# Kernel optimization log

Hardware: AMD Instinct MI355X
Metric: run time of the kernel (lower is better)

Reference implementation:

```python
import jax, jax.numpy as jnp
import numpy as np

D, H, DH, R = 1024, 16, 64, 32          # embed, heads, head_dim, per-head attn rank
R_OUT, I, R_FC1, R_FC2 = 512, 4096, 512, 512
B, S = 2, 2048
EPS = 1e-5


def _layernorm(x, w, b):
    m = jnp.mean(x, axis=-1, keepdims=True)
    v = jnp.mean(jnp.square(x - m), axis=-1, keepdims=True)
    return (x - m) * jax.lax.rsqrt(v + EPS) * w + b


def setup_inputs() -> dict:
    key = jax.random.key(0)
    ks = jax.random.split(key, 24)
    n = lambda i, shape, s: (jax.random.normal(ks[i], shape, jnp.float32) * s)
    return {
        'hidden_states': jax.random.normal(ks[0], (B, S, D), jnp.float32),
        'attention_mask': jnp.ones((B, S), dtype=bool),
        'ln1_w': jnp.ones((D,), jnp.float32), 'ln1_b': jnp.zeros((D,), jnp.float32),
        'q_U': n(1, (D, H, R), 0.02), 'q_V': n(2, (H, R, DH), 0.1), 'q_b': jnp.zeros((H, DH), jnp.float32),
        'k_U': n(3, (D, H, R), 0.02), 'k_V': n(4, (H, R, DH), 0.1), 'k_b': jnp.zeros((H, DH), jnp.float32),
        'v_U': n(5, (D, H, R), 0.02), 'v_V': n(6, (H, R, DH), 0.1), 'v_b': jnp.zeros((H, DH), jnp.float32),
        'out_U': n(7, (D, R_OUT), 0.02), 'out_V': n(8, (R_OUT, D), 0.02), 'out_b': jnp.zeros((D,), jnp.float32),
        'ln2_w': jnp.ones((D,), jnp.float32), 'ln2_b': jnp.zeros((D,), jnp.float32),
        'fc1_U': n(9, (D, R_FC1), 0.02), 'fc1_V': n(10, (R_FC1, I), 0.02), 'fc1_b': jnp.zeros((I,), jnp.float32),
        'fc2_U': n(11, (I, R_FC2), 0.02), 'fc2_V': n(12, (R_FC2, D), 0.02), 'fc2_b': jnp.zeros((D,), jnp.float32),
    }


def _forward(hidden_states, attention_mask, ln1_w, ln1_b, q_U, q_V, q_b, k_U, k_V, k_b,
             v_U, v_V, v_b, out_U, out_V, out_b, ln2_w, ln2_b,
             fc1_U, fc1_V, fc1_b, fc2_U, fc2_V, fc2_b):
    b, s, d = hidden_states.shape
    x = _layernorm(hidden_states, ln1_w, ln1_b)
    # low-rank per-head projections: P = x U  (bhsr), then Q = P V + b
    Pq = jnp.einsum('bsd,dhr->bhsr', x, q_U)
    Pk = jnp.einsum('bsd,dhr->bhsr', x, k_U)
    Pv = jnp.einsum('bsd,dhr->bhsr', x, v_U)
    Q = jnp.einsum('bhsr,hre->bhse', Pq, q_V) + q_b[None, :, None, :]
    K = jnp.einsum('bhsr,hre->bhse', Pk, k_V) + k_b[None, :, None, :]
    V = jnp.einsum('bhsr,hre->bhse', Pv, v_V) + v_b[None, :, None, :]
    scale = 1.0 / jnp.sqrt(jnp.asarray(DH, Q.dtype))
    scores = jnp.einsum('bhse,bhte->bhst', Q, K) * scale
    causal = jnp.tril(jnp.ones((s, s), dtype=bool))
    keymask = attention_mask[:, None, None, :]  # [B,1,1,S] key padding mask
    mask = jnp.logical_and(causal[None, None], keymask)
    scores = jnp.where(mask, scores, jnp.asarray(-1e9, scores.dtype))
    P = jax.nn.softmax(scores, axis=-1)
    Y = jnp.einsum('bhst,bhte->bhse', P, V)           # [B,H,S,dh]
    Y = Y.transpose(0, 2, 1, 3).reshape(b, s, d)       # [B,S,D]
    Y = (Y @ out_U) @ out_V + out_b                    # low-rank out-proj
    h = hidden_states + Y
    z = _layernorm(h, ln2_w, ln2_b)
    t1 = z @ fc1_U                                     # [B,S,r_fc1]
    a = jax.nn.gelu(t1 @ fc1_V + fc1_b, approximate=True)
    h2 = (a @ fc2_U) @ fc2_V + fc2_b
    return h + h2


def reference(hidden_states, attention_mask, ln1_w, ln1_b, q_U, q_V, q_b, k_U, k_V, k_b,
              v_U, v_V, v_b, out_U, out_V, out_b, ln2_w, ln2_b,
              fc1_U, fc1_V, fc1_b, fc2_U, fc2_V, fc2_b):
    return _forward(hidden_states, attention_mask, ln1_w, ln1_b, q_U, q_V, q_b,
                    k_U, k_V, k_b, v_U, v_V, v_b, out_U, out_V, out_b,
                    ln2_w, ln2_b, fc1_U, fc1_V, fc1_b, fc2_U, fc2_V, fc2_b)
```

## Files before the change

kernel.cpp:

```cpp
#include <hip/hip_runtime.h>
#include <math.h>

constexpr int Bc = 2, Sc = 2048, Dc = 1024, Hc = 16, DHc = 64, Rc = 32;
constexpr int Nt = Bc * Sc;
constexpr int NP3 = 1536;

typedef __attribute__((ext_vector_type(8))) short bf16x8;
typedef __attribute__((ext_vector_type(4))) float f32x4;

__device__ __forceinline__ unsigned short f2bf(float f) {
  unsigned u = __float_as_uint(f);
  u += 0x7fffu + ((u >> 16) & 1u);
  return (unsigned short)(u >> 16);
}
__device__ __forceinline__ float bf2f(unsigned short h) {
  return __uint_as_float(((unsigned)h) << 16);
}

#define GLOAD_LDS16(gp, lp)                                                    \
  __builtin_amdgcn_global_load_lds(                                            \
      (const __attribute__((address_space(1))) void*)(gp),                     \
      (__attribute__((address_space(3))) void*)(lp), 16, 0, 0)

__global__ __launch_bounds__(256) void ln_kernel(
    const float* __restrict__ X, const float* __restrict__ w,
    const float* __restrict__ b, unsigned short* __restrict__ Out) {
  int row = blockIdx.x;
  const float* x = X + (size_t)row * Dc;
  unsigned short* o = Out + (size_t)row * Dc;
  int tid = threadIdx.x;
  float4 v = ((const float4*)x)[tid];
  float s  = v.x + v.y + v.z + v.w;
  float sq = v.x * v.x + v.y * v.y + v.z * v.z + v.w * v.w;
#pragma unroll
  for (int off = 32; off; off >>= 1) {
    s  += __shfl_down(s, off);
    sq += __shfl_down(sq, off);
  }
  __shared__ float rs[4], rq[4];
  int wid = tid >> 6, lane = tid & 63;
  if (lane == 0) { rs[wid] = s; rq[wid] = sq; }
  __syncthreads();
  float ts = rs[0] + rs[1] + rs[2] + rs[3];
  float tq = rq[0] + rq[1] + rq[2] + rq[3];
  float mean = ts * (1.f / Dc);
  float var  = tq * (1.f / Dc) - mean * mean;
  float rstd = rsqrtf(var + 1e-5f);
  float4 wv = ((const float4*)w)[tid];
  float4 bv = ((const float4*)b)[tid];
  ushort4 ov;
  ov.x = f2bf((v.x - mean) * rstd * wv.x + bv.x);
  ov.y = f2bf((v.y - mean) * rstd * wv.y + bv.y);
  ov.z = f2bf((v.z - mean) * rstd * wv.z + bv.z);
  ov.w = f2bf((v.w - mean) * rstd * wv.w + bv.w);
  ((ushort4*)o)[tid] = ov;
}

__global__ __launch_bounds__(256) void transpose_cvt(
    const float* __restrict__ in, unsigned short* __restrict__ out,
    int R, int C) {
  __shared__ float t[32][33];
  int tx = threadIdx.x & 31, ty = threadIdx.x >> 5;
  int r0 = blockIdx.y * 32, c0 = blockIdx.x * 32;
#pragma unroll
  for (int i = 0; i < 4; ++i)
    t[ty + i * 8][tx] = in[(size_t)(r0 + ty + i * 8) * C + c0 + tx];
  __syncthreads();
#pragma unroll
  for (int i = 0; i < 4; ++i)
    out[(size_t)(c0 + ty + i * 8) * R + r0 + tx] = f2bf(t[tx][ty + i * 8]);
}

__global__ __launch_bounds__(256) void transpose_hd(
    const unsigned short* __restrict__ in, unsigned short* __restrict__ out) {
  __shared__ unsigned short t[32][33];
  int bh = blockIdx.z;
  int s0 = blockIdx.x * 32, e0 = blockIdx.y * 32;
  int tx = threadIdx.x & 31, ty = threadIdx.x >> 5;
  const unsigned short* ib = in + ((size_t)bh * Sc + s0) * 64 + e0;
  unsigned short* ob = out + ((size_t)bh * 64 + e0) * Sc + s0;
#pragma unroll
  for (int i = 0; i < 4; ++i)
    t[ty + i * 8][tx] = ib[(size_t)(ty + i * 8) * 64 + tx];
  __syncthreads();
#pragma unroll
  for (int i = 0; i < 4; ++i)
    ob[(size_t)(ty + i * 8) * Sc + tx] = t[tx][ty + i * 8];
}

__device__ __forceinline__ float gelu_f(float v) {
  float c = v + 0.044715f * v * v * v;
  return 0.5f * v * (1.f + tanhf(0.7978845608028654f * c));
}

template <bool OBF16, int ACT, bool BIAS, bool RES>
__global__ __launch_bounds__(256) void gemm_bf(
    const unsigned short* __restrict__ A, const unsigned short* __restrict__ BT,
    const float* __restrict__ bias, const float* __restrict__ res,
    void* __restrict__ Cv, int M, int N, int K) {
  __shared__ unsigned short As[128 * 32];
  __shared__ unsigned short Bs[128 * 32];
  int tid = threadIdx.x;
  int lane = tid & 63, wv = tid >> 6;
  int bm = blockIdx.y * 128, bn = blockIdx.x * 128;
  int wr = wv >> 1, wc = wv & 1;
  f32x4 acc[4][4] = {};
  int soff0 = wv * 512 + lane * 8;
  int soff1 = soff0 + 2048;
  int ar0 = soff0 >> 5, ak0 = soff0 & 31;
  int ar1 = soff1 >> 5, ak1 = soff1 & 31;
  const unsigned short* Ab = A + (size_t)bm * K;
  const unsigned short* Bb = BT + (size_t)bn * K;
  for (int k0 = 0; k0 < K; k0 += 32) {
    __syncthreads();
    GLOAD_LDS16(Ab + (size_t)ar0 * K + k0 + ak0, As + wv * 512);
    GLOAD_LDS16(Ab + (size_t)ar1 * K + k0 + ak1, As + 2048 + wv * 512);
    GLOAD_LDS16(Bb + (size_t)ar0 * K + k0 + ak0, Bs + wv * 512);
    GLOAD_LDS16(Bb + (size_t)ar1 * K + k0 + ak1, Bs + 2048 + wv * 512);
    __syncthreads();
    bf16x8 af[4], bf[4];
#pragma unroll
    for (int m = 0; m < 4; ++m)
      af[m] = *(const bf16x8*)&As[(wr * 64 + m * 16 + (lane & 15)) * 32 + (lane >> 4) * 8];
#pragma unroll
    for (int n = 0; n < 4; ++n)
      bf[n] = *(const bf16x8*)&Bs[(wc * 64 + n * 16 + (lane & 15)) * 32 + (lane >> 4) * 8];
#pragma unroll
    for (int m = 0; m < 4; ++m)
#pragma unroll
      for (int n = 0; n < 4; ++n)
        acc[m][n] = __builtin_amdgcn_mfma_f32_16x16x32_bf16(af[m], bf[n], acc[m][n], 0, 0, 0);
  }
  int cg = lane >> 4;
#pragma unroll
  for (int m = 0; m < 4; ++m) {
#pragma unroll
    for (int n = 0; n < 4; ++n) {
      int row0 = bm + wr * 64 + m * 16 + cg * 4;
      int col  = bn + wc * 64 + n * 16 + (lane & 15);
      float bb = BIAS ? bias[col] : 0.f;
#pragma unroll
      for (int i = 0; i < 4; ++i) {
        float v = acc[m][n][i];
        if (BIAS) v += bb;
        if (ACT == 1) v = gelu_f(v);
        if (RES) v += res[(size_t)(row0 + i) * N + col];
        if (OBF16)
          ((unsigned short*)Cv)[(size_t)(row0 + i) * N + col] = f2bf(v);
        else
          ((float*)Cv)[(size_t)(row0 + i) * N + col] = v;
      }
    }
  }
}

__global__ __launch_bounds__(256) void pv_kernel(
    const unsigned short* __restrict__ P, const float* __restrict__ Vw,
    const float* __restrict__ bias, unsigned short* __restrict__ Out,
    int colOff) {
  int idx = blockIdx.x * 256 + threadIdx.x;
  int e = idx & 63;
  int h = (idx >> 6) & 15;
  int n = idx >> 10;
  const unsigned short* prow = P + (size_t)n * NP3 + colOff + h * Rc;
  const float* vcol = Vw + h * (Rc * DHc) + e;
  float acc = 0.f;
#pragma unroll
  for (int r = 0; r < Rc; ++r) acc = fmaf(bf2f(prow[r]), vcol[r * DHc], acc);
  acc += bias[(h << 6) + e];
  int b = n / Sc, s = n % Sc;
  Out[(((size_t)(b * Hc + h) * Sc + s) << 6) + e] = f2bf(acc);
}

__global__ __launch_bounds__(256) void attn_kernel(
    const unsigned short* __restrict__ Q, const unsigned short* __restrict__ K,
    const unsigned short* __restrict__ VT, unsigned short* __restrict__ Y) {
  __shared__ unsigned short Ks[64 * 64];
  __shared__ unsigned short Vs[64 * 64];
  __shared__ unsigned short Ps[4][16 * 64];
  int bid = blockIdx.x;
  int bh = bid >> 5;
  int qt = 31 - (bid & 31);
  int qbase = qt * 64;
  int tid = threadIdx.x, lane = tid & 63, w = tid >> 6;
  int g = lane >> 4, c = lane & 15;
  const unsigned short* Qg = Q + (size_t)bh * Sc * 64;
  const unsigned short* Kg = K + (size_t)bh * Sc * 64;
  const unsigned short* Vg = VT + (size_t)bh * 64 * Sc;
  int q0 = qbase + w * 16;
  bf16x8 qa0 = *(const bf16x8*)(Qg + (size_t)(q0 + c) * 64 + g * 8);
  bf16x8 qa1 = *(const bf16x8*)(Qg + (size_t)(q0 + c) * 64 + 32 + g * 8);
  f32x4 O0 = {0.f, 0.f, 0.f, 0.f}, O1 = O0, O2 = O0, O3 = O0;
  float m[4] = {-1e30f, -1e30f, -1e30f, -1e30f};
  float l[4] = {0.f, 0.f, 0.f, 0.f};
  int r0s = tid >> 3;
  int b0s = (tid & 7) ^ (r0s & 7);
  int r1s = (256 + tid) >> 3;
  int b1s = (tid & 7) ^ (r1s & 7);
  size_t kOff0 = (size_t)r0s * 64 + b0s * 8;
  size_t kOff1 = (size_t)r1s * 64 + b1s * 8;
  size_t vOff0 = (size_t)r0s * Sc + b0s * 8;
  size_t vOff1 = (size_t)r1s * Sc + b1s * 8;
  unsigned short* KsD0 = Ks + w * 512;
  unsigned short* KsD1 = Ks + 2048 + w * 512;
  unsigned short* VsD0 = Vs + w * 512;
  unsigned short* VsD1 = Vs + 2048 + w * 512;
  unsigned short* Pw = Ps[w];
  const f32x4 zero = {0.f, 0.f, 0.f, 0.f};
  int swc = c & 7;

  for (int kt = 0; kt <= qt; ++kt) {
    __syncthreads();
    {
      const unsigned short* Kt = Kg + (size_t)kt * 64 * 64;
      const unsigned short* Vt = Vg + (size_t)kt * 64;
      GLOAD_LDS16(Kt + kOff0, KsD0);
      GLOAD_LDS16(Kt + kOff1, KsD1);
      GLOAD_LDS16(Vt + vOff0, VsD0);
      GLOAD_LDS16(Vt + vOff1, VsD1);
    }
    __syncthreads();
    f32x4 sA[4];
#pragma unroll
    for (int kb = 0; kb < 4; ++kb) {
      int keyr = kb * 16 + c;
      int sw = keyr & 7;
      bf16x8 k0 = *(const bf16x8*)&Ks[keyr * 64 + ((g ^ sw) << 3)];
      bf16x8 k1 = *(const bf16x8*)&Ks[keyr * 64 + (((4 + g) ^ sw) << 3)];
      f32x4 a = __builtin_amdgcn_mfma_f32_16x16x32_bf16(qa0, k0, zero, 0, 0, 0);
      a = __builtin_amdgcn_mfma_f32_16x16x32_bf16(qa1, k1, a, 0, 0, 0);
      sA[kb] = a;
    }
    float p[4][4], rm[4];
#pragma unroll
    for (int i = 0; i < 4; ++i) rm[i] = -1e30f;
#pragma unroll
    for (int kb = 0; kb < 4; ++kb)
#pragma unroll
      for (int i = 0; i < 4; ++i) {
        float s = sA[kb][i] * 0.125f;
        if (kt == qt && (kb * 16 + c) > (w * 16 + 4 * g + i)) s = -1e30f;
        p[kb][i] = s;
        rm[i] = fmaxf(rm[i], s);
      }
#pragma unroll
    for (int i = 0; i < 4; ++i) {
      rm[i] = fmaxf(rm[i], __shfl_xor(rm[i], 1));
      rm[i] = fmaxf(rm[i], __shfl_xor(rm[i], 2));
      rm[i] = fmaxf(rm[i], __shfl_xor(rm[i], 4));
      rm[i] = fmaxf(rm[i], __shfl_xor(rm[i], 8));
    }
    float sc[4], ls[4];
#pragma unroll
    for (int i = 0; i < 4; ++i) {
      float mn = fmaxf(m[i], rm[i]);
      sc[i] = __expf(m[i] - mn);
      m[i] = mn;
      ls[i] = 0.f;
    }
#pragma unroll
    for (int kb = 0; kb < 4; ++kb)
#pragma unroll
      for (int i = 0; i < 4; ++i) {
        float e = __expf(p[kb][i] - m[i]);
        p[kb][i] = e;
        ls[i] += e;
      }
#pragma unroll
    for (int i = 0; i < 4; ++i) {
      ls[i] += __shfl_xor(ls[i], 1);
      ls[i] += __shfl_xor(ls[i], 2);
      ls[i] += __shfl_xor(ls[i], 4);
      ls[i] += __shfl_xor(ls[i], 8);
      l[i] = l[i] * sc[i] + ls[i];
      O0[i] *= sc[i]; O1[i] *= sc[i]; O2[i] *= sc[i]; O3[i] *= sc[i];
    }
#pragma unroll
    for (int kb = 0; kb < 4; ++kb)
#pragma unroll
      for (int i = 0; i < 4; ++i) {
        int row = 4 * g + i;
        int slot = (kb * 2 + (c >> 3)) ^ (row & 7);
        Pw[row * 64 + slot * 8 + (c & 7)] = f2bf(p[kb][i]);
      }
    bf16x8 pa0 = *(const bf16x8*)&Pw[c * 64 + ((g ^ swc) << 3)];
    bf16x8 pa1 = *(const bf16x8*)&Pw[c * 64 + (((4 + g) ^ swc) << 3)];
#define PV_DB(db, Ov)                                                          \
    {                                                                          \
      int d_ = db * 16 + c;                                                    \
      bf16x8 v0 = *(const bf16x8*)&Vs[d_ * 64 + ((g ^ swc) << 3)];             \
      bf16x8 v1 = *(const bf16x8*)&Vs[d_ * 64 + (((4 + g) ^ swc) << 3)];       \
      Ov = __builtin_amdgcn_mfma_f32_16x16x32_bf16(pa0, v0, Ov, 0, 0, 0);      \
      Ov = __builtin_amdgcn_mfma_f32_16x16x32_bf16(pa1, v1, Ov, 0, 0, 0);      \
    }
    PV_DB(0, O0) PV_DB(1, O1) PV_DB(2, O2) PV_DB(3, O3)
#undef PV_DB
  }
  float inv[4];
#pragma unroll
  for (int i = 0; i < 4; ++i) inv[i] = 1.f / l[i];
  int b = bh >> 4, h = bh & 15;
#define WR_DB(db, Ov)                                                          \
  {                                                                            \
    _Pragma("unroll")                                                          \
    for (int i = 0; i < 4; ++i) {                                              \
      int q_ = q0 + 4 * g + i;                                                 \
      Y[(size_t)(b * Sc + q_) * Dc + h * 64 + db * 16 + c] =                   \
          f2bf(Ov[i] * inv[i]);                                                \
    }                                                                          \
  }
  WR_DB(0, O0) WR_DB(1, O1) WR_DB(2, O2) WR_DB(3, O3)
#undef WR_DB
}

extern "C" void kernel_launch(void* const* d_in, const int* in_sizes, int n_in,
                              void* d_out, int out_size, void* d_ws, size_t ws_size,
                              hipStream_t stream) {
  const float* hidden = (const float*)d_in[0];
  const float* ln1_w = (const float*)d_in[2];
  const float* ln1_b = (const float*)d_in[3];
  const float* q_U = (const float*)d_in[4];
  const float* q_V = (const float*)d_in[5];
  const float* q_b = (const float*)d_in[6];
  const float* k_U = (const float*)d_in[7];
  const float* k_V = (const float*)d_in[8];
  const float* k_b = (const float*)d_in[9];
  const float* v_U = (const float*)d_in[10];
  const float* v_V = (const float*)d_in[11];
  const float* v_b = (const float*)d_in[12];
  const float* out_U = (const float*)d_in[13];
  const float* out_V = (const float*)d_in[14];
  const float* out_b = (const float*)d_in[15];
  const float* ln2_w = (const float*)d_in[16];
  const float* ln2_b = (const float*)d_in[17];
  const float* fc1_U = (const float*)d_in[18];
  const float* fc1_V = (const float*)d_in[19];
  const float* fc1_b = (const float*)d_in[20];
  const float* fc2_U = (const float*)d_in[21];
  const float* fc2_V = (const float*)d_in[22];
  const float* fc2_b = (const float*)d_in[23];
  float* out = (float*)d_out;

  char* wsb = (char*)d_ws;
  auto US = [&](size_t mb) { return (unsigned short*)(wsb + mb * 1024 * 1024); };
  unsigned short* WqkvT = US(0);
  unsigned short* outUT = US(3);
  unsigned short* outVT = US(4);
  unsigned short* fc1UT = US(5);
  unsigned short* fc1VT = US(6);
  unsigned short* fc2UT = US(10);
  unsigned short* fc2VT = US(14);
  unsigned short* xb    = US(15);
  unsigned short* Pqkv  = US(23);
  unsigned short* Vt    = US(23);
  unsigned short* Qb    = US(35);
  unsigned short* Kb    = US(43);
  unsigned short* Vb    = US(51);
  unsigned short* Yb    = US(59);
  unsigned short* Tb    = US(67);
  float*          hb    = (float*)(wsb + 71ull * 1024 * 1024);
  unsigned short* ab    = US(87);

  transpose_cvt<<<dim3(512 / 32, 1024 / 32), 256, 0, stream>>>(q_U, WqkvT, 1024, 512);
  transpose_cvt<<<dim3(512 / 32, 1024 / 32), 256, 0, stream>>>(k_U, WqkvT + 512 * 1024, 1024, 512);
  transpose_cvt<<<dim3(512 / 32, 1024 / 32), 256, 0, stream>>>(v_U, WqkvT + 1024 * 1024, 1024, 512);
  transpose_cvt<<<dim3(512 / 32, 1024 / 32), 256, 0, stream>>>(out_U, outUT, 1024, 512);
  transpose_cvt<<<dim3(1024 / 32, 512 / 32), 256, 0, stream>>>(out_V, outVT, 512, 1024);
  transpose_cvt<<<dim3(512 / 32, 1024 / 32), 256, 0, stream>>>(fc1_U, fc1UT, 1024, 512);
  transpose_cvt<<<dim3(4096 / 32, 512 / 32), 256, 0, stream>>>(fc1_V, fc1VT, 512, 4096);
  transpose_cvt<<<dim3(512 / 32, 4096 / 32), 256, 0, stream>>>(fc2_U, fc2UT, 4096, 512);
  transpose_cvt<<<dim3(1024 / 32, 512 / 32), 256, 0, stream>>>(fc2_V, fc2VT, 512, 1024);

  ln_kernel<<<Nt, 256, 0, stream>>>(hidden, ln1_w, ln1_b, xb);
  gemm_bf<true, 0, false, false><<<dim3(NP3 / 128, Nt / 128), 256, 0, stream>>>(
      xb, WqkvT, nullptr, nullptr, Pqkv, Nt, NP3, Dc);
  int pvBlocks = Nt * Hc * DHc / 256;
  pv_kernel<<<pvBlocks, 256, 0, stream>>>(Pqkv, q_V, q_b, Qb, 0);
  pv_kernel<<<pvBlocks, 256, 0, stream>>>(Pqkv, k_V, k_b, Kb, 512);
  pv_kernel<<<pvBlocks, 256, 0, stream>>>(Pqkv, v_V, v_b, Vb, 1024);
  transpose_hd<<<dim3(Sc / 32, 2, Bc * Hc), 256, 0, stream>>>(Vb, Vt);
  attn_kernel<<<Bc * Hc * (Sc / 64), 256, 0, stream>>>(Qb, Kb, Vt, Yb);
  gemm_bf<true, 0, false, false><<<dim3(512 / 128, Nt / 128), 256, 0, stream>>>(
      Yb, outUT, nullptr, nullptr, Tb, Nt, 512, Dc);
  gemm_bf<false, 0, true, true><<<dim3(Dc / 128, Nt / 128), 256, 0, stream>>>(
      Tb, outVT, out_b, hidden, hb, Nt, Dc, 512);
  ln_kernel<<<Nt, 256, 0, stream>>>(hb, ln2_w, ln2_b, xb);
  gemm_bf<true, 0, false, false><<<dim3(512 / 128, Nt / 128), 256, 0, stream>>>(
      xb, fc1UT, nullptr, nullptr, Tb, Nt, 512, Dc);
  gemm_bf<true, 1, true, false><<<dim3(4096 / 128, Nt / 128), 256, 0, stream>>>(
      Tb, fc1VT, fc1_b, nullptr, ab, Nt, 4096, 512);
  gemm_bf<true, 0, false, false><<<dim3(512 / 128, Nt / 128), 256, 0, stream>>>(
      ab, fc2UT, nullptr, nullptr, Tb, Nt, 512, 4096);
  gemm_bf<false, 0, true, true><<<dim3(Dc / 128, Nt / 128), 256, 0, stream>>>(
      Tb, fc2VT, fc2_b, hb, out, Nt, Dc, 512);
}
```

Baseline: 597.0 us.

## Double-buffer attention K/V tiles, add 128x64 GEMM tile, fuse QKV rank-up launches

The attention kernel now keeps two LDS buffers for K and V. It issues the async global-to-LDS loads for the next key tile before computing on the current one, so one barrier per iteration replaces two and the loads can overlap compute. A new 128x64-tile GEMM variant is used for the three N=512 low-rank projections. This doubles the block count for those launches so more compute units are occupied, at the cost of less reuse of the A tile per block. The three per-head rank-up kernels for Q, K and V are merged into one launch indexed by blockIdx.y, which removes launch overhead.

```diff
diff --git a/kernel.cpp b/kernel.cpp
--- a/kernel.cpp
+++ b/kernel.cpp
@@ -154,10 +154,77 @@
   }
 }
 
-__global__ __launch_bounds__(256) void pv_kernel(
-    const unsigned short* __restrict__ P, const float* __restrict__ Vw,
-    const float* __restrict__ bias, unsigned short* __restrict__ Out,
-    int colOff) {
+template <bool OBF16, int ACT, bool BIAS, bool RES>
+__global__ __launch_bounds__(256) void gemm_bf_n64(
+    const unsigned short* __restrict__ A, const unsigned short* __restrict__ BT,
+    const float* __restrict__ bias, const float* __restrict__ res,
+    void* __restrict__ Cv, int M, int N, int K) {
+  __shared__ unsigned short As[128 * 32];
+  __shared__ unsigned short Bs[64 * 32];
+  int tid = threadIdx.x;
+  int lane = tid & 63, wv = tid >> 6;
+  int bm = blockIdx.y * 128, bn = blockIdx.x * 64;
+  f32x4 acc[2][4] = {};
+  int soff0 = wv * 512 + lane * 8;
+  int soff1 = soff0 + 2048;
+  int ar0 = soff0 >> 5, ak0 = soff0 & 31;
+  int ar1 = soff1 >> 5, ak1 = soff1 & 31;
+  const unsigned short* Ab = A + (size_t)bm * K;
+  const unsigned short* Bb = BT + (size_t)bn * K;
+  int c = lane & 15, g = lane >> 4;
+  for (int k0 = 0; k0 < K; k0 += 32) {
+    __syncthreads();
+    GLOAD_LDS16(Ab + (size_t)ar0 * K + k0 + ak0, As + wv * 512);
+    GLOAD_LDS16(Ab + (size_t)ar1 * K + k0 + ak1, As + 2048 + wv * 512);
+    GLOAD_LDS16(Bb + (size_t)ar0 * K + k0 + ak0, Bs + wv * 512);
+    __syncthreads();
+    bf16x8 af[2], bfr[4];
+#pragma unroll
+    for (int m = 0; m < 2; ++m)
+      af[m] = *(const bf16x8*)&As[(wv * 32 + m * 16 + c) * 32 + g * 8];
+#pragma unroll
+    for (int n = 0; n < 4; ++n)
+      bfr[n] = *(const bf16x8*)&Bs[(n * 16 + c) * 32 + g * 8];
+#pragma unroll
+    for (int m = 0; m < 2; ++m)
+#pragma unroll
+      for (int n = 0; n < 4; ++n)
+        acc[m][n] = __builtin_amdgcn_mfma_f32_16x16x32_bf16(af[m], bfr[n], acc[m][n], 0, 0, 0);
+  }
+#pragma unroll
+  for (int m = 0; m < 2; ++m) {
+#pragma unroll
+    for (int n = 0; n < 4; ++n) {
+      int row0 = bm + wv * 32 + m * 16 + g * 4;
+      int col  = bn + n * 16 + c;
+      float bb = BIAS ? bias[col] : 0.f;
+#pragma unroll
+      for (int i = 0; i < 4; ++i) {
+        float v = acc[m][n][i];
+        if (BIAS) v += bb;
+        if (ACT == 1) v = gelu_f(v);
+        if (RES) v += res[(size_t)(row0 + i) * N + col];
+        if (OBF16)
+          ((unsigned short*)Cv)[(size_t)(row0 + i) * N + col] = f2bf(v);
+        else
+          ((float*)Cv)[(size_t)(row0 + i) * N + col] = v;
+      }
+    }
+  }
+}
+
+__global__ __launch_bounds__(256) void pv3_kernel(
+    const unsigned short* __restrict__ P,
+    const float* __restrict__ qV, const float* __restrict__ kV,
+    const float* __restrict__ vV, const float* __restrict__ qb,
+    const float* __restrict__ kb, const float* __restrict__ vb,
+    unsigned short* __restrict__ Qb, unsigned short* __restrict__ Kb,
+    unsigned short* __restrict__ Vb) {
+  int which = blockIdx.y;
+  const float* Vw = which == 0 ? qV : which == 1 ? kV : vV;
+  const float* bias = which == 0 ? qb : which == 1 ? kb : vb;
+  unsigned short* Out = which == 0 ? Qb : which == 1 ? Kb : Vb;
+  int colOff = which * 512;
   int idx = blockIdx.x * 256 + threadIdx.x;
   int e = idx & 63;
   int h = (idx >> 6) & 15;
@@ -175,8 +242,8 @@
 __global__ __launch_bounds__(256) void attn_kernel(
     const unsigned short* __restrict__ Q, const unsigned short* __restrict__ K,
     const unsigned short* __restrict__ VT, unsigned short* __restrict__ Y) {
-  __shared__ unsigned short Ks[64 * 64];
-  __shared__ unsigned short Vs[64 * 64];
+  __shared__ unsigned short Ks[2][64 * 64];
+  __shared__ unsigned short Vs[2][64 * 64];
   __shared__ unsigned short Ps[4][16 * 64];
   int bid = blockIdx.x;
   int bh = bid >> 5;
@@ -201,32 +268,35 @@
   size_t kOff1 = (size_t)r1s * 64 + b1s * 8;
   size_t vOff0 = (size_t)r0s * Sc + b0s * 8;
   size_t vOff1 = (size_t)r1s * Sc + b1s * 8;
-  unsigned short* KsD0 = Ks + w * 512;
-  unsigned short* KsD1 = Ks + 2048 + w * 512;
-  unsigned short* VsD0 = Vs + w * 512;
-  unsigned short* VsD1 = Vs + 2048 + w * 512;
   unsigned short* Pw = Ps[w];
   const f32x4 zero = {0.f, 0.f, 0.f, 0.f};
   int swc = c & 7;
-
+  int wOff = w * 512;
+
+#define STAGE(kt_, buf_)                                                       \
+  {                                                                            \
+    const unsigned short* Kt_ = Kg + (size_t)(kt_) * 64 * 64;                  \
+    const unsigned short* Vt_ = Vg + (size_t)(kt_) * 64;                       \
+    GLOAD_LDS16(Kt_ + kOff0, &Ks[buf_][wOff]);                                 \
+    GLOAD_LDS16(Kt_ + kOff1, &Ks[buf_][2048 + wOff]);                          \
+    GLOAD_LDS16(Vt_ + vOff0, &Vs[buf_][wOff]);                                 \
+    GLOAD_LDS16(Vt_ + vOff1, &Vs[buf_][2048 + wOff]);                          \
+  }
+
+  STAGE(0, 0);
   for (int kt = 0; kt <= qt; ++kt) {
+    int buf = kt & 1;
     __syncthreads();
-    {
-      const unsigned short* Kt = Kg + (size_t)kt * 64 * 64;
-      const unsigned short* Vt = Vg + (size_t)kt * 64;
-      GLOAD_LDS16(Kt + kOff0, KsD0);
-      GLOAD_LDS16(Kt + kOff1, KsD1);
-      GLOAD_LDS16(Vt + vOff0, VsD0);
-      GLOAD_LDS16(Vt + vOff1, VsD1);
-    }
-    __syncthreads();
+    if (kt < qt) STAGE(kt + 1, buf ^ 1);
+    const unsigned short* Ksb = Ks[buf];
+    const unsigned short* Vsb = Vs[buf];
     f32x4 sA[4];
 #pragma unroll
     for (int kb = 0; kb < 4; ++kb) {
       int keyr = kb * 16 + c;
       int sw = keyr & 7;
-      bf16x8 k0 = *(const bf16x8*)&Ks[keyr * 64 + ((g ^ sw) << 3)];
-      bf16x8 k1 = *(const bf16x8*)&Ks[keyr * 64 + (((4 + g) ^ sw) << 3)];
+      bf16x8 k0 = *(const bf16x8*)&Ksb[keyr * 64 + ((g ^ sw) << 3)];
+      bf16x8 k1 = *(const bf16x8*)&Ksb[keyr * 64 + (((4 + g) ^ sw) << 3)];
       f32x4 a = __builtin_amdgcn_mfma_f32_16x16x32_bf16(qa0, k0, zero, 0, 0, 0);
       a = __builtin_amdgcn_mfma_f32_16x16x32_bf16(qa1, k1, a, 0, 0, 0);
       sA[kb] = a;
@@ -288,14 +358,15 @@
 #define PV_DB(db, Ov)                                                          \
     {                                                                          \
       int d_ = db * 16 + c;                                                    \
-      bf16x8 v0 = *(const bf16x8*)&Vs[d_ * 64 + ((g ^ swc) << 3)];             \
-      bf16x8 v1 = *(const bf16x8*)&Vs[d_ * 64 + (((4 + g) ^ swc) << 3)];       \
+      bf16x8 v0 = *(const bf16x8*)&Vsb[d_ * 64 + ((g ^ swc) << 3)];            \
+      bf16x8 v1 = *(const bf16x8*)&Vsb[d_ * 64 + (((4 + g) ^ swc) << 3)];      \
       Ov = __builtin_amdgcn_mfma_f32_16x16x32_bf16(pa0, v0, Ov, 0, 0, 0);      \
       Ov = __builtin_amdgcn_mfma_f32_16x16x32_bf16(pa1, v1, Ov, 0, 0, 0);      \
     }
     PV_DB(0, O0) PV_DB(1, O1) PV_DB(2, O2) PV_DB(3, O3)
 #undef PV_DB
   }
+#undef STAGE
   float inv[4];
 #pragma unroll
   for (int i = 0; i < 4; ++i) inv[i] = 1.f / l[i];
@@ -375,21 +446,20 @@
   gemm_bf<true, 0, false, false><<<dim3(NP3 / 128, Nt / 128), 256, 0, stream>>>(
       xb, WqkvT, nullptr, nullptr, Pqkv, Nt, NP3, Dc);
   int pvBlocks = Nt * Hc * DHc / 256;
-  pv_kernel<<<pvBlocks, 256, 0, stream>>>(Pqkv, q_V, q_b, Qb, 0);
-  pv_kernel<<<pvBlocks, 256, 0, stream>>>(Pqkv, k_V, k_b, Kb, 512);
-  pv_kernel<<<pvBlocks, 256, 0, stream>>>(Pqkv, v_V, v_b, Vb, 1024);
+  pv3_kernel<<<dim3(pvBlocks, 3), 256, 0, stream>>>(
+      Pqkv, q_V, k_V, v_V, q_b, k_b, v_b, Qb, Kb, Vb);
   transpose_hd<<<dim3(Sc / 32, 2, Bc * Hc), 256, 0, stream>>>(Vb, Vt);
   attn_kernel<<<Bc * Hc * (Sc / 64), 256, 0, stream>>>(Qb, Kb, Vt, Yb);
-  gemm_bf<true, 0, false, false><<<dim3(512 / 128, Nt / 128), 256, 0, stream>>>(
+  gemm_bf_n64<true, 0, false, false><<<dim3(512 / 64, Nt / 128), 256, 0, stream>>>(
       Yb, outUT, nullptr, nullptr, Tb, Nt, 512, Dc);
   gemm_bf<false, 0, true, true><<<dim3(Dc / 128, Nt / 128), 256, 0, stream>>>(
       Tb, outVT, out_b, hidden, hb, Nt, Dc, 512);
   ln_kernel<<<Nt, 256, 0, stream>>>(hb, ln2_w, ln2_b, xb);
-  gemm_bf<true, 0, false, false><<<dim3(512 / 128, Nt / 128), 256, 0, stream>>>(
+  gemm_bf_n64<true, 0, false, false><<<dim3(512 / 64, Nt / 128), 256, 0, stream>>>(
       xb, fc1UT, nullptr, nullptr, Tb, Nt, 512, Dc);
   gemm_bf<true, 1, true, false><<<dim3(4096 / 128, Nt / 128), 256, 0, stream>>>(
       Tb, fc1VT, fc1_b, nullptr, ab, Nt, 4096, 512);
-  gemm_bf<true, 0, false, false><<<dim3(512 / 128, Nt / 128), 256, 0, stream>>>(
+  gemm_bf_n64<true, 0, false, false><<<dim3(512 / 64, Nt / 128), 256, 0, stream>>>(
       ab, fc2UT, nullptr, nullptr, Tb, Nt, 512, 4096);
   gemm_bf<false, 0, true, true><<<dim3(Dc / 128, Nt / 128), 256, 0, stream>>>(
       Tb, fc2VT, fc2_b, hb, out, Nt, Dc, 512);
```

Result: faster. 557.4 us (-6.6%).
